# Kernel optimization log

Hardware: AMD Instinct MI355X
Metric: run time of the kernel (lower is better)

## Reference

```python
import jax, jax.numpy as jnp
import numpy as np

B, N, E, H, KVC = 2, 1024, 512, 8, 1536  # KVC = 3*E, head_dim = E//H = 64
EPS = 1e-5  # torch InstanceNorm2d default eps


def instance_norm(x):
    # normalize over the last two (spatial) dims per (batch, channel); biased var, no affine
    mu = jnp.mean(x, axis=(-2, -1), keepdims=True)
    var = jnp.var(x, axis=(-2, -1), keepdims=True)
    return (x - mu) * jax.lax.rsqrt(var + EPS)


def _heads(x):
    # [B, T, E] -> [B, H, T, E//H]
    b, t, e = x.shape
    return x.reshape(b, t, H, e // H).transpose(0, 2, 1, 3)


def setup_inputs() -> dict:
    key = jax.random.key(0)
    ks = jax.random.split(key, 16)
    s_e = 1.0 / np.sqrt(E)
    s_c = 1.0 / np.sqrt(KVC)
    inp = {
        'emb1': jax.random.normal(ks[0], (B, N, E), jnp.float32),
        'emb2': jax.random.normal(ks[1], (B, N, E), jnp.float32),
        'emb3': jax.random.normal(ks[2], (B, N, E), jnp.float32),
        'emb_C': jax.random.normal(ks[3], (B, N, KVC), jnp.float32),
        'Wq1': jax.random.normal(ks[4], (E, E), jnp.float32) * s_e,
        'Wq2': jax.random.normal(ks[5], (E, E), jnp.float32) * s_e,
        'Wq3': jax.random.normal(ks[6], (E, E), jnp.float32) * s_e,
        'Wk': jax.random.normal(ks[7], (E, E), jnp.float32) * s_e,
        'Wv': jax.random.normal(ks[8], (E, E), jnp.float32) * s_e,
        'WqC': jax.random.normal(ks[9], (KVC, KVC), jnp.float32) * s_c,
        'WkC': jax.random.normal(ks[10], (KVC, KVC), jnp.float32) * s_c,
        'WvC': jax.random.normal(ks[11], (KVC, KVC), jnp.float32) * s_c,
        'Wo1': jax.random.normal(ks[12], (E, E), jnp.float32) * s_e,
        'Wo2': jax.random.normal(ks[13], (E, E), jnp.float32) * s_e,
        'Wo3': jax.random.normal(ks[14], (E, E), jnp.float32) * s_e,
    }
    return inp


def reference(emb1, emb2, emb3, emb_C, Wq1, Wq2, Wq3, Wk, Wv, WqC, WkC, WvC, Wo1, Wo2, Wo3):
    # ---- channel attention over emb_C ----
    Q_C = emb_C @ WqC.T  # [B, N, KVC]
    K_C = emb_C @ WkC.T
    V_C = emb_C @ WvC.T
    attn_c = jnp.einsum('bnc,bnd->bcd', Q_C, K_C)          # [B, KVC, KVC]
    ch_sim = jax.nn.softmax(instance_norm(attn_c), axis=-1)  # psi1 (1 channel) + softmax(dim=3)
    ctx_c = jnp.einsum('bcd,bnd->bcn', ch_sim, V_C)        # [B, KVC, N]
    T_hat = ctx_c.transpose(0, 2, 1)                        # [B, N, KVC]
    # split last dim into 3 chunks of E, concat along token dim -> shared K/V source [B, 3N, E]
    KV_S = jnp.concatenate(jnp.split(T_hat, 3, axis=2), axis=1)

    # ---- spatial attention: 3 query streams share one K/V ----
    K = _heads(KV_S @ Wk.T)                # [B, H, 3N, d]
    V = _heads(KV_S @ Wv.T)                # [B, H, 3N, d]
    Kt = K.transpose(0, 1, 3, 2)           # [B, H, d, 3N]

    def stream(emb, Wq, Wo):
        Q = _heads(emb @ Wq.T)              # [B, H, N, d]
        attn = Q @ Kt                       # [B, H, N, 3N]
        sim = jax.nn.softmax(instance_norm(attn), axis=-1)  # psi2 per (b,h) + softmax
        ctx = sim @ V                       # [B, H, N, d]
        ctx = ctx.transpose(0, 2, 1, 3).reshape(emb.shape[0], emb.shape[1], E)
        return ctx @ Wo.T

    O1 = stream(emb1, Wq1, Wo1)
    O2 = stream(emb2, Wq2, Wo2)
    O3 = stream(emb3, Wq3, Wo3)
    return (O1, O2, O3)
```

## Files before the change

### kernel.cpp

```cpp
#include <hip/hip_runtime.h>
#include <math.h>

#define NTOK 1024
#define EDIM 512
#define KVCH 1536
#define TKV  3072
#define VSTRIDE 6144

typedef __bf16 bf16x8 __attribute__((ext_vector_type(8)));
typedef float f32x4 __attribute__((ext_vector_type(4)));
#define MFMA16(a,b,c) __builtin_amdgcn_mfma_f32_16x16x32_bf16(a,b,c,0,0,0)

__device__ __forceinline__ ushort f2bf(float f){
    uint u = __float_as_uint(f);
    u += 0x7FFFu + ((u>>16)&1u);
    return (ushort)(u>>16);
}
__device__ __forceinline__ float bf2f(ushort h){ return __uint_as_float(((uint)h)<<16); }
__device__ __forceinline__ bf16x8 ldsb8(const ushort* p){ return *(const bf16x8*)p; }

__device__ __forceinline__ void async16(const ushort* g, ushort* l){
    __builtin_amdgcn_global_load_lds((const __attribute__((address_space(1))) void*)g,
                                     (__attribute__((address_space(3))) void*)l, 16, 0, 0);
}

#define NCVT 15
struct CvtJobs { const float* src[NCVT]; ushort* hi[NCVT]; ushort* lo[NCVT]; int n[NCVT]; };

__global__ __launch_bounds__(256) void cvt_hilo(CvtJobs J)
{
    int a = blockIdx.y;
    int i = (blockIdx.x*256 + threadIdx.x)*4;
    if (i >= J.n[a]) return;
    float4 v = *(const float4*)(J.src[a] + i);
    ushort4 h, l;
    h.x=f2bf(v.x); l.x=f2bf(v.x-bf2f(h.x));
    h.y=f2bf(v.y); l.y=f2bf(v.y-bf2f(h.y));
    h.z=f2bf(v.z); l.z=f2bf(v.z-bf2f(h.z));
    h.w=f2bf(v.w); l.w=f2bf(v.w-bf2f(h.w));
    *(ushort4*)(J.hi[a]+i) = h;
    *(ushort4*)(J.lo[a]+i) = l;
}

struct GemmDesc {
    const ushort *Ahi, *Alo, *Bhi, *Blo;
    float* Cf; ushort *Chi, *Clo, *Cthi, *Ctlo;
    double* stats;
    int K, lda, ldb, ldc, ldct;
    int zmod;
    long sA0, sA1, sB0, sB1, sC0, sC1;
};

__device__ __forceinline__ void stage_ab(const ushort* hi, const ushort* lo, int ld, int k0,
                                         ushort* lds, int wave, int lane)
{
    #pragma unroll
    for (int i=0;i<4;++i){
        int r = (i<<5) + (wave<<3) + (lane>>3);
        int g = (lane&7) ^ (r&7);
        const ushort* s = ((g&4) ? lo : hi) + (size_t)r*ld + k0 + ((g&3)<<3);
        async16(s, lds + (((i<<5) + (wave<<3))<<6));
    }
}

__global__ __launch_bounds__(256) void mgemmF(GemmDesc D0, GemmDesc D1,
                                              int nblk0, int nx0, int ny0, int nx1, int ny1)
{
    __shared__ ushort A2[2][8192], B2[2][8192];
    __shared__ double sred[8];
    const int tid = threadIdx.x;
    int bid = blockIdx.x;
    GemmDesc d; int nx, ny, rel;
    if (bid < nblk0) { d = D0; rel = bid; nx = nx0; ny = ny0; }
    else             { d = D1; rel = bid - nblk0; nx = nx1; ny = ny1; }
    const int bx = rel % nx; int tt = rel / nx;
    const int by = tt % ny;  const int z = tt / ny;
    const int zb = z / d.zmod, zj = z - zb*d.zmod;
    const int mb = by<<7, nb = bx<<7;
    const ushort* Ah = d.Ahi + (size_t)zb*d.sA0 + (size_t)zj*d.sA1 + (size_t)mb*d.lda;
    const ushort* Al = d.Alo + (size_t)zb*d.sA0 + (size_t)zj*d.sA1 + (size_t)mb*d.lda;
    const ushort* Bh = d.Bhi + (size_t)zb*d.sB0 + (size_t)zj*d.sB1 + (size_t)nb*d.ldb;
    const ushort* Bl = d.Blo + (size_t)zb*d.sB0 + (size_t)zj*d.sB1 + (size_t)nb*d.ldb;
    const size_t coff = (size_t)zb*d.sC0 + (size_t)zj*d.sC1;
    const int wave = tid>>6, lane = tid&63;
    const int wr = wave>>1, wc = wave&1;
    const int fr = lane&15, fq = lane>>4;
    f32x4 acc[4][4];
    #pragma unroll
    for (int i=0;i<4;++i)
        #pragma unroll
        for (int j=0;j<4;++j) acc[i][j] = (f32x4){0.f,0.f,0.f,0.f};

    stage_ab(Ah, Al, d.lda, 0, A2[0], wave, lane);
    stage_ab(Bh, Bl, d.ldb, 0, B2[0], wave, lane);
    __syncthreads();
    int cur = 0;
    for (int k0=0; k0<d.K; k0+=32) {
        if (k0+32 < d.K) {
            stage_ab(Ah, Al, d.lda, k0+32, A2[cur^1], wave, lane);
            stage_ab(Bh, Bl, d.ldb, k0+32, B2[cur^1], wave, lane);
        }
        bf16x8 fah[4], fal[4];
        #pragma unroll
        for (int m=0;m<4;++m) {
            int r = wr*64 + m*16 + fr;
            const ushort* base = &A2[cur][r<<6];
            fah[m] = ldsb8(base + ((fq ^ (r&7))<<3));
            fal[m] = ldsb8(base + (((fq|4) ^ (r&7))<<3));
        }
        #pragma unroll
        for (int n=0;n<4;++n) {
            int r = wc*64 + n*16 + fr;
            const ushort* base = &B2[cur][r<<6];
            bf16x8 fbh = ldsb8(base + ((fq ^ (r&7))<<3));
            bf16x8 fbl = ldsb8(base + (((fq|4) ^ (r&7))<<3));
            #pragma unroll
            for (int m=0;m<4;++m) {
                acc[m][n] = MFMA16(fah[m], fbh, acc[m][n]);
                acc[m][n] = MFMA16(fah[m], fbl, acc[m][n]);
                acc[m][n] = MFMA16(fal[m], fbh, acc[m][n]);
            }
        }
        __syncthreads();
        cur ^= 1;
    }
    #pragma unroll
    for (int m=0;m<4;++m) {
        #pragma unroll
        for (int n=0;n<4;++n) {
            int row = mb + wr*64 + m*16 + fq*4;
            int col = nb + wc*64 + n*16 + fr;
            f32x4 v = acc[m][n];
            if (d.Cf) {
                #pragma unroll
                for (int r=0;r<4;++r) d.Cf[coff + (size_t)(row+r)*d.ldc + col] = v[r];
            }
            if (d.Chi) {
                #pragma unroll
                for (int r=0;r<4;++r) {
                    ushort hh = f2bf(v[r]);
                    size_t o = coff + (size_t)(row+r)*d.ldc + col;
                    d.Chi[o] = hh; d.Clo[o] = f2bf(v[r]-bf2f(hh));
                }
            }
            if (d.Cthi) {
                ushort4 h4, l4;
                #pragma unroll
                for (int r=0;r<4;++r) {
                    ushort hh = f2bf(v[r]);
                    ((ushort*)&h4)[r] = hh;
                    ((ushort*)&l4)[r] = f2bf(v[r]-bf2f(hh));
                }
                size_t o = coff + (size_t)col*d.ldct + row;
                *(ushort4*)(d.Cthi+o) = h4;
                *(ushort4*)(d.Ctlo+o) = l4;
            }
        }
    }
    if (d.stats) {
        double s=0.0, s2=0.0;
        #pragma unroll
        for (int m=0;m<4;++m)
            #pragma unroll
            for (int n=0;n<4;++n)
                #pragma unroll
                for (int r=0;r<4;++r) { double v = acc[m][n][r]; s += v; s2 += v*v; }
        #pragma unroll
        for (int off=32; off; off>>=1) { s += __shfl_xor(s, off); s2 += __shfl_xor(s2, off); }
        if (lane==0){ sred[wave]=s; sred[4+wave]=s2; }
        __syncthreads();
        if (tid==0) {
            atomicAdd(&d.stats[2*zb],   sred[0]+sred[1]+sred[2]+sred[3]);
            atomicAdd(&d.stats[2*zb+1], sred[4]+sred[5]+sred[6]+sred[7]);
        }
    }
}

__global__ __launch_bounds__(256) void chan_softmax(const float* __restrict__ ATT, const double* __restrict__ ST,
                                                    ushort* __restrict__ Shi, ushort* __restrict__ Slo)
{
    int b = blockIdx.y;
    size_t ro = (size_t)b * KVCH * KVCH + (size_t)blockIdx.x * KVCH;
    const float* p = ATT + ro;
    ushort* ph = Shi + ro;
    ushort* pl = Slo + ro;
    double cnt = (double)KVCH * (double)KVCH;
    double mean = ST[2*b] / cnt;
    double var  = ST[2*b+1] / cnt - mean * mean;
    float sc = (float)(1.0 / sqrt(var + 1e-5));
    int tid = threadIdx.x;
    float x[6];
    #pragma unroll
    for (int k = 0; k < 6; ++k) x[k] = p[tid + (k << 8)] * sc;
    float mx = fmaxf(fmaxf(fmaxf(x[0],x[1]),fmaxf(x[2],x[3])),fmaxf(x[4],x[5]));
    #pragma unroll
    for (int m = 32; m; m >>= 1) mx = fmaxf(mx, __shfl_xor(mx, m));
    __shared__ float red[4];
    int w = tid >> 6;
    if ((tid & 63) == 0) red[w] = mx;
    __syncthreads();
    mx = fmaxf(fmaxf(red[0],red[1]), fmaxf(red[2],red[3]));
    __syncthreads();
    float e[6]; float sum = 0.f;
    #pragma unroll
    for (int k = 0; k < 6; ++k) { e[k] = __expf(x[k] - mx); sum += e[k]; }
    #pragma unroll
    for (int m = 32; m; m >>= 1) sum += __shfl_xor(sum, m);
    if ((tid & 63) == 0) red[w] = sum;
    __syncthreads();
    sum = red[0]+red[1]+red[2]+red[3];
    float inv = 1.0f / sum;
    #pragma unroll
    for (int k = 0; k < 6; ++k) {
        float pv = e[k] * inv;
        ushort hh = f2bf(pv);
        ph[tid + (k << 8)] = hh;
        pl[tid + (k << 8)] = f2bf(pv - bf2f(hh));
    }
}

__global__ __launch_bounds__(256) void gram4(
    const ushort* __restrict__ Kbhi, const ushort* __restrict__ Kblo,
    const ushort* __restrict__ QBhi, const ushort* __restrict__ QBlo,
    float* __restrict__ GK, float* __restrict__ SK,
    float* __restrict__ GQ, float* __restrict__ SQm)
{
    int z = blockIdx.z;
    const ushort *Xh, *Xl; int T; float *G, *CS;
    if (z == 0) { Xh=Kbhi; Xl=Kblo; T=TKV; G=GK; CS=SK; }
    else { Xh=QBhi+(size_t)(z-1)*1048576; Xl=QBlo+(size_t)(z-1)*1048576;
           T=NTOK; G=GQ+(size_t)(z-1)*65536; CS=SQm+(size_t)(z-1)*1024; }
    int bh = blockIdx.x;
    int b = bh >> 3, h = bh & 7;
    const ushort* Xbh = Xh + (size_t)b * T * EDIM + h * 64;
    const ushort* Xbl = Xl + (size_t)b * T * EDIM + h * 64;
    int rows = T / gridDim.y;
    int t0 = blockIdx.y * rows;
    __shared__ float Xs[4][64];
    int tid = threadIdx.x;
    int i0 = (tid >> 4) << 2, j0 = (tid & 15) << 2;
    float acc[4][4] = {};
    float cs = 0.f;
    for (int t = t0; t < t0 + rows; t += 4) {
        __syncthreads();
        int r = tid >> 6, c = tid & 63;
        size_t gidx = (size_t)(t + r) * EDIM + c;
        Xs[r][c] = bf2f(Xbh[gidx]) + bf2f(Xbl[gidx]);
        __syncthreads();
        #pragma unroll
        for (int rr = 0; rr < 4; ++rr) {
            float xi0=Xs[rr][i0], xi1=Xs[rr][i0+1], xi2=Xs[rr][i0+2], xi3=Xs[rr][i0+3];
            float xj0=Xs[rr][j0], xj1=Xs[rr][j0+1], xj2=Xs[rr][j0+2], xj3=Xs[rr][j0+3];
            acc[0][0]=fmaf(xi0,xj0,acc[0][0]); acc[0][1]=fmaf(xi0,xj1,acc[0][1]); acc[0][2]=fmaf(xi0,xj2,acc[0][2]); acc[0][3]=fmaf(xi0,xj3,acc[0][3]);
            acc[1][0]=fmaf(xi1,xj0,acc[1][0]); acc[1][1]=fmaf(xi1,xj1,acc[1][1]); acc[1][2]=fmaf(xi1,xj2,acc[1][2]); acc[1][3]=fmaf(xi1,xj3,acc[1][3]);
            acc[2][0]=fmaf(xi2,xj0,acc[2][0]); acc[2][1]=fmaf(xi2,xj1,acc[2][1]); acc[2][2]=fmaf(xi2,xj2,acc[2][2]); acc[2][3]=fmaf(xi2,xj3,acc[2][3]);
            acc[3][0]=fmaf(xi3,xj0,acc[3][0]); acc[3][1]=fmaf(xi3,xj1,acc[3][1]); acc[3][2]=fmaf(xi3,xj2,acc[3][2]); acc[3][3]=fmaf(xi3,xj3,acc[3][3]);
        }
        if (tid < 64) cs += Xs[0][tid] + Xs[1][tid] + Xs[2][tid] + Xs[3][tid];
    }
    float* Gp = G + (size_t)bh * 4096;
    #pragma unroll
    for (int i = 0; i < 4; ++i)
        #pragma unroll
        for (int j = 0; j < 4; ++j)
            atomicAdd(&Gp[(i0 + i) * 64 + j0 + j], acc[i][j]);
    if (tid < 64) atomicAdd(&CS[bh * 64 + tid], cs);
}

__global__ __launch_bounds__(256) void spatial_scale(
    const float* __restrict__ GQ, const float* __restrict__ GK,
    const float* __restrict__ SQm, const float* __restrict__ SKm, float* __restrict__ SVo)
{
    int st = blockIdx.y, bh = blockIdx.x, tid = threadIdx.x;
    const float* gq = GQ + (size_t)st*65536 + bh*4096;
    const float* gk = GK + bh*4096;
    double e2 = 0.0;
    for (int i = tid; i < 4096; i += 256)
        e2 += (double)gq[i] * (double)gk[i];
    double mm = 0.0;
    if (tid < 64) mm = (double)SQm[(size_t)st*1024 + bh*64 + tid] * (double)SKm[bh*64 + tid];
    #pragma unroll
    for (int m = 32; m; m >>= 1) { e2 += __shfl_xor(e2, m); mm += __shfl_xor(mm, m); }
    __shared__ double se[4], sm[4];
    int w = tid >> 6;
    if ((tid & 63) == 0) { se[w] = e2; sm[w] = mm; }
    __syncthreads();
    if (tid == 0) {
        double cnt = (double)NTOK * (double)TKV;
        double E2 = (se[0]+se[1]+se[2]+se[3]) / cnt;
        double M  = (sm[0]+sm[1]+sm[2]+sm[3]) / cnt;
        double var = E2 - M * M;
        SVo[st*16+bh] = (float)(1.0 / sqrt(var + 1e-5));
    }
}

__global__ __launch_bounds__(256) void flash_mfma(
    const ushort* __restrict__ Qhi, const ushort* __restrict__ Qlo,
    const ushort* __restrict__ Khi, const ushort* __restrict__ Klo,
    const ushort* __restrict__ VThi, const ushort* __restrict__ VTlo,
    const float* __restrict__ SV,
    ushort* __restrict__ Ohi, ushort* __restrict__ Olo)
{
    __shared__ ushort Kh[2][4096], Kl[2][4096], Vh[2][4096], Vl[2][4096], Ph[4096];
    const int st = blockIdx.z, bh = blockIdx.y, b = bh>>3, h = bh&7;
    const int n0 = blockIdx.x<<6;
    const int tid = threadIdx.x, wave = tid>>6, lane = tid&63;
    const int fr = lane&15, fq = lane>>4;
    const float sc = SV[st*16 + bh];
    const size_t qb = (size_t)st*1048576 + (size_t)(b*1024 + n0)*512 + h*64;
    bf16x8 qfh[2], qfl[2];
    {
        const ushort* qph = Qhi + qb + (size_t)(wave*16 + fr)*512;
        const ushort* qpl = Qlo + qb + (size_t)(wave*16 + fr)*512;
        #pragma unroll
        for (int ks=0; ks<2; ++ks) {
            qfh[ks] = ldsb8(qph + ks*32 + fq*8);
            qfl[ks] = ldsb8(qpl + ks*32 + fq*8);
        }
    }
    f32x4 accO[4]; float lsum[4];
    #pragma unroll
    for (int i=0;i<4;++i){ accO[i]=(f32x4){0.f,0.f,0.f,0.f}; lsum[i]=0.f; }
    const size_t kb = (size_t)(b*TKV)*512 + h*64;
    const size_t vb = (size_t)(h*64)*VSTRIDE + b*TKV;

    auto stage_kv = [&](int tn, int buf){
        #pragma unroll
        for (int it=0; it<2; ++it) {
            int r  = (wave<<4) + (it<<3) + (lane>>3);
            int lb = ((wave<<4) + (it<<3)) << 6;
            int gck = ((lane&7) ^ (r&7)) << 3;
            size_t gk = kb + (size_t)(tn+r)*512 + gck;
            size_t gv = vb + (size_t)r*VSTRIDE + tn + gck;
            async16(Khi+gk, &Kh[buf][lb]);
            async16(Klo+gk, &Kl[buf][lb]);
            async16(VThi+gv, &Vh[buf][lb]);
            async16(VTlo+gv, &Vl[buf][lb]);
        }
    };

    stage_kv(0, 0);
    __syncthreads();
    int cur = 0;
    for (int t0=0; t0<TKV; t0+=64) {
        if (t0+64 < TKV) stage_kv(t0+64, cur^1);
        f32x4 s[4];
        #pragma unroll
        for (int i=0;i<4;++i) s[i]=(f32x4){0.f,0.f,0.f,0.f};
        #pragma unroll
        for (int ks=0; ks<2; ++ks) {
            #pragma unroll
            for (int nf=0; nf<4; ++nf) {
                int r = nf*16+fr;
                int ko = (r<<6) + ((ks*32 + fq*8) ^ ((r&7)<<3));
                bf16x8 kh = ldsb8(&Kh[cur][ko]), kl = ldsb8(&Kl[cur][ko]);
                s[nf] = MFMA16(qfh[ks], kh, s[nf]);
                s[nf] = MFMA16(qfh[ks], kl, s[nf]);
                s[nf] = MFMA16(qfl[ks], kh, s[nf]);
            }
        }
        #pragma unroll
        for (int reg=0; reg<4; ++reg) {
            int prow = fq*4+reg;
            float psum = 0.f;
            #pragma unroll
            for (int nf=0;nf<4;++nf){
                float p = __expf(sc * s[nf][reg]);
                psum += p;
                int pidx = (wave<<10) + (prow<<6) + ((nf*16+fr) ^ ((prow&7)<<3));
                Ph[pidx] = f2bf(p);
            }
            lsum[reg] += psum;
        }
        #pragma unroll
        for (int ks=0; ks<2; ++ks) {
            int po = (wave<<10) + (fr<<6) + ((ks*32 + fq*8) ^ ((fr&7)<<3));
            bf16x8 ph = ldsb8(&Ph[po]);
            #pragma unroll
            for (int df=0; df<4; ++df) {
                int dd = df*16+fr;
                int vo = (dd<<6) + ((ks*32 + fq*8) ^ ((dd&7)<<3));
                bf16x8 vh = ldsb8(&Vh[cur][vo]), vl = ldsb8(&Vl[cur][vo]);
                accO[df] = MFMA16(ph, vh, accO[df]);
                accO[df] = MFMA16(ph, vl, accO[df]);
            }
        }
        __syncthreads();
        cur ^= 1;
    }
    #pragma unroll
    for (int reg=0; reg<4; ++reg) {
        #pragma unroll
        for (int m=1; m<16; m<<=1) lsum[reg] += __shfl_xor(lsum[reg], m, 16);
        float inv = 1.f/lsum[reg];
        int row = n0 + wave*16 + fq*4 + reg;
        #pragma unroll
        for (int df=0; df<4; ++df) {
            float v = accO[df][reg]*inv;
            size_t o = (size_t)st*1048576 + (size_t)(b*1024+row)*512 + h*64 + df*16 + fr;
            ushort hh = f2bf(v);
            Ohi[o] = hh; Olo[o] = f2bf(v-bf2f(hh));
        }
    }
}

constexpr size_t OFF_CH  = 0;
constexpr size_t OFF_GK  = 64;
constexpr size_t OFF_SK  = 262208;
constexpr size_t OFF_GQ  = 266304;
constexpr size_t OFF_SQM = 1052736;
constexpr size_t OFF_SV  = 1065024;
constexpr size_t ZERO_BYTES = 1065024;
constexpr size_t S0 = 1065472;
constexpr size_t S1 = S0 + 8388608;
constexpr size_t S2 = S1 + 28311552;
constexpr size_t S3 = S2 + 12582912;
constexpr size_t S4 = S3 + 12582912;
constexpr size_t S5 = S4 + 12582912;
constexpr size_t S6 = S5 + 12582912;

extern "C" void kernel_launch(void* const* d_in, const int* in_sizes, int n_in,
                              void* d_out, int out_size, void* d_ws, size_t ws_size,
                              hipStream_t stream)
{
    const float* emb[3] = {(const float*)d_in[0], (const float*)d_in[1], (const float*)d_in[2]};
    const float* embC = (const float*)d_in[3];
    const float* WqF[3] = {(const float*)d_in[4], (const float*)d_in[5], (const float*)d_in[6]};
    const float* WkF  = (const float*)d_in[7];
    const float* WvF  = (const float*)d_in[8];
    const float* WCF[3] = {(const float*)d_in[9], (const float*)d_in[10], (const float*)d_in[11]};
    const float* WoF[3] = {(const float*)d_in[12], (const float*)d_in[13], (const float*)d_in[14]};
    float* out = (float*)d_out;
    char* ws = (char*)d_ws;

    auto U16 = [&](size_t off)->ushort* { return (ushort*)(ws + off); };
    auto F32 = [&](size_t off)->float*  { return (float*)(ws + off); };

    double* CH = (double*)(ws + OFF_CH);
    float *GK = F32(OFF_GK), *SK = F32(OFF_SK), *GQ = F32(OFF_GQ), *SQm = F32(OFF_SQM), *SV = F32(OFF_SV);

    auto W8hi = [&](int i){ return U16(S0 + (size_t)i*1048576); };
    auto W8lo = [&](int i){ return U16(S0 + (size_t)i*1048576 + 524288); };
    auto WChi = [&](int i){ return U16(S1 + (size_t)i*9437184); };
    auto WClo = [&](int i){ return U16(S1 + (size_t)i*9437184 + 4718592); };
    ushort *embChi=U16(S2), *embClo=U16(S2+6291456);
    ushort *embhi=U16(S3), *emblo=U16(S3+6291456);
    ushort *QCthi=U16(S4), *QCtlo=U16(S4+6291456);
    ushort *KCthi=U16(S5), *KCtlo=U16(S5+6291456);
    ushort *VChi=U16(S6), *VClo=U16(S6+6291456);
    float  *ATT = F32(S1);
    ushort *SIMhi=U16(S4), *SIMlo=U16(S4+9437184);
    ushort *KVShi=U16(S2), *KVSlo=U16(S2+6291456);
    ushort *QBhi=U16(S1), *QBlo=U16(S1+6291456);
    ushort *Kbhi=U16(S1+12582912), *Kblo=U16(S1+12582912+6291456);
    ushort *VThi=U16(S6), *VTlo=U16(S6+6291456);
    ushort *CTXhi=U16(S5), *CTXlo=U16(S5+6291456);

    dim3 blk(256);
    (void)hipMemsetAsync(d_ws, 0, ZERO_BYTES, stream);

    CvtJobs J;
    J.src[0]=embC;   J.hi[0]=embChi; J.lo[0]=embClo; J.n[0]=2048*KVCH;
    for (int s=0;s<3;++s){ J.src[1+s]=emb[s]; J.hi[1+s]=embhi+(size_t)s*1048576; J.lo[1+s]=emblo+(size_t)s*1048576; J.n[1+s]=2*NTOK*EDIM; }
    for (int s=0;s<3;++s){ J.src[4+s]=WqF[s]; J.hi[4+s]=W8hi(s); J.lo[4+s]=W8lo(s); J.n[4+s]=EDIM*EDIM; }
    J.src[7]=WkF; J.hi[7]=W8hi(3); J.lo[7]=W8lo(3); J.n[7]=EDIM*EDIM;
    J.src[8]=WvF; J.hi[8]=W8hi(4); J.lo[8]=W8lo(4); J.n[8]=EDIM*EDIM;
    for (int s=0;s<3;++s){ J.src[9+s]=WCF[s]; J.hi[9+s]=WChi(s); J.lo[9+s]=WClo(s); J.n[9+s]=KVCH*KVCH; }
    for (int s=0;s<3;++s){ J.src[12+s]=WoF[s]; J.hi[12+s]=W8hi(5+s); J.lo[12+s]=W8lo(5+s); J.n[12+s]=EDIM*EDIM; }
    cvt_hilo<<<dim3(3072, NCVT), blk, 0, stream>>>(J);

    GemmDesc Z{}; Z.zmod = 1;

    {
        GemmDesc dq = Z;
        dq.Ahi=embChi; dq.Alo=embClo; dq.Bhi=WChi(0); dq.Blo=WClo(0);
        dq.Cthi=QCthi; dq.Ctlo=QCtlo;
        dq.K=KVCH; dq.lda=KVCH; dq.ldb=KVCH; dq.ldct=NTOK;
        dq.zmod=2; dq.sA0=0; dq.sA1=(long)NTOK*KVCH; dq.sB0=4718592; dq.sB1=0;
        dq.sC0=6291456; dq.sC1=(long)KVCH*NTOK;
        GemmDesc dv = Z;
        dv.Ahi=embChi; dv.Alo=embClo; dv.Bhi=WChi(2); dv.Blo=WClo(2);
        dv.Chi=VChi; dv.Clo=VClo;
        dv.K=KVCH; dv.lda=KVCH; dv.ldb=KVCH; dv.ldc=KVCH;
        dv.sA0=(long)NTOK*KVCH; dv.sC0=(long)NTOK*KVCH;
        mgemmF<<<dim3(576), blk, 0, stream>>>(dq, dv, 384, 12, 8, 12, 8);
    }
    {
        GemmDesc da = Z;
        da.Ahi=QCthi; da.Alo=QCtlo; da.Bhi=KCthi; da.Blo=KCtlo;
        da.Cf=ATT; da.stats=CH;
        da.K=NTOK; da.lda=NTOK; da.ldb=NTOK; da.ldc=KVCH;
        da.sA0=(long)KVCH*NTOK; da.sB0=(long)KVCH*NTOK; da.sC0=(long)KVCH*KVCH;
        mgemmF<<<dim3(288), blk, 0, stream>>>(da, da, 288, 12, 12, 1, 1);
    }
    chan_softmax<<<dim3(1536,2), blk, 0, stream>>>(ATT, CH, SIMhi, SIMlo);
    {
        GemmDesc dk = Z;
        dk.Ahi=VChi; dk.Alo=VClo; dk.Bhi=SIMhi; dk.Blo=SIMlo;
        dk.Chi=KVShi; dk.Clo=KVSlo;
        dk.K=KVCH; dk.lda=KVCH; dk.ldb=KVCH; dk.ldc=EDIM;
        dk.zmod=3; dk.sA0=(long)NTOK*KVCH; dk.sA1=0;
        dk.sB0=(long)KVCH*KVCH; dk.sB1=(long)EDIM*KVCH;
        dk.sC0=(long)TKV*EDIM; dk.sC1=(long)NTOK*EDIM;
        GemmDesc dqp = Z;
        dqp.Ahi=embhi; dqp.Alo=emblo; dqp.Bhi=W8hi(0); dqp.Blo=W8lo(0);
        dqp.Chi=QBhi; dqp.Clo=QBlo;
        dqp.K=EDIM; dqp.lda=EDIM; dqp.ldb=EDIM; dqp.ldc=EDIM;
        dqp.sA0=1048576; dqp.sB0=524288; dqp.sC0=1048576;
        mgemmF<<<dim3(384), blk, 0, stream>>>(dk, dqp, 192, 4, 8, 4, 16);
    }
    {
        GemmDesc dkp = Z;
        dkp.Ahi=KVShi; dkp.Alo=KVSlo; dkp.Bhi=W8hi(3); dkp.Blo=W8lo(3);
        dkp.Chi=Kbhi; dkp.Clo=Kblo;
        dkp.K=EDIM; dkp.lda=EDIM; dkp.ldb=EDIM; dkp.ldc=EDIM;
        GemmDesc dvp = Z;
        dvp.Ahi=KVShi; dvp.Alo=KVSlo; dvp.Bhi=W8hi(4); dvp.Blo=W8lo(4);
        dvp.Cthi=VThi; dvp.Ctlo=VTlo;
        dvp.K=EDIM; dvp.lda=EDIM; dvp.ldb=EDIM; dvp.ldct=VSTRIDE;
        mgemmF<<<dim3(384), blk, 0, stream>>>(dkp, dvp, 192, 4, 48, 4, 48);
    }
    gram4<<<dim3(16,8,4), blk, 0, stream>>>(Kbhi, Kblo, QBhi, QBlo, GK, SK, GQ, SQm);
    spatial_scale<<<dim3(16,3), blk, 0, stream>>>(GQ, GK, SQm, SK, SV);
    flash_mfma<<<dim3(16,16,3), blk, 0, stream>>>(QBhi, QBlo, Kbhi, Kblo, VThi, VTlo, SV, CTXhi, CTXlo);
    {
        GemmDesc dop = Z;
        dop.Ahi=CTXhi; dop.Alo=CTXlo; dop.Bhi=W8hi(5); dop.Blo=W8lo(5);
        dop.Cf=out;
        dop.K=EDIM; dop.lda=EDIM; dop.ldb=EDIM; dop.ldc=EDIM;
        dop.sA0=1048576; dop.sB0=524288; dop.sC0=1048576;
        mgemmF<<<dim3(192), blk, 0, stream>>>(dop, dop, 192, 4, 16, 1, 1);
    }
}
```

Baseline: 684.0 us.

## Single-buffer flash KV tiles, remap blocks per XCD, raise MFMA wave priority

The flash attention kernel drops its double-buffered K/V LDS staging for a single buffer with a barrier after each load. This halves LDS use so more blocks can be resident per CU, and relies on occupancy rather than software prefetch to hide load latency. The grid becomes 1-D and is remapped so that blocks landing on the same XCD share the same (stream, batch, head) K/V data, which is meant to improve L2 reuse. s_setprio is raised around the MFMA sections in both the flash and GEMM kernels. In exchange, loads inside each block are no longer overlapped with compute.

```diff
diff --git a/kernel.cpp b/kernel.cpp
--- a/kernel.cpp
+++ b/kernel.cpp
@@ -108,6 +108,7 @@
             fah[m] = ldsb8(base + ((fq ^ (r&7))<<3));
             fal[m] = ldsb8(base + (((fq|4) ^ (r&7))<<3));
         }
+        __builtin_amdgcn_s_setprio(1);
         #pragma unroll
         for (int n=0;n<4;++n) {
             int r = wc*64 + n*16 + fr;
@@ -121,6 +122,7 @@
                 acc[m][n] = MFMA16(fal[m], fbh, acc[m][n]);
             }
         }
+        __builtin_amdgcn_s_setprio(0);
         __syncthreads();
         cur ^= 1;
     }
@@ -301,9 +303,13 @@
     const float* __restrict__ SV,
     ushort* __restrict__ Ohi, ushort* __restrict__ Olo)
 {
-    __shared__ ushort Kh[2][4096], Kl[2][4096], Vh[2][4096], Vl[2][4096], Ph[4096];
-    const int st = blockIdx.z, bh = blockIdx.y, b = bh>>3, h = bh&7;
-    const int n0 = blockIdx.x<<6;
+    __shared__ ushort Kh[4096], Kl[4096], Vh[4096], Vl[4096], Ph[4096];
+    const int g = blockIdx.x;
+    const int xcd = g & 7, loc = g >> 3;
+    const int sbh = xcd*6 + (loc >> 4);
+    const int st = sbh >> 4, bh = sbh & 15;
+    const int b = bh>>3, h = bh&7;
+    const int n0 = (loc & 15) << 6;
     const int tid = threadIdx.x, wave = tid>>6, lane = tid&63;
     const int fr = lane&15, fq = lane>>4;
     const float sc = SV[st*16 + bh];
@@ -323,42 +329,37 @@
     for (int i=0;i<4;++i){ accO[i]=(f32x4){0.f,0.f,0.f,0.f}; lsum[i]=0.f; }
     const size_t kb = (size_t)(b*TKV)*512 + h*64;
     const size_t vb = (size_t)(h*64)*VSTRIDE + b*TKV;
-
-    auto stage_kv = [&](int tn, int buf){
+    for (int t0=0; t0<TKV; t0+=64) {
         #pragma unroll
         for (int it=0; it<2; ++it) {
             int r  = (wave<<4) + (it<<3) + (lane>>3);
             int lb = ((wave<<4) + (it<<3)) << 6;
             int gck = ((lane&7) ^ (r&7)) << 3;
-            size_t gk = kb + (size_t)(tn+r)*512 + gck;
-            size_t gv = vb + (size_t)r*VSTRIDE + tn + gck;
-            async16(Khi+gk, &Kh[buf][lb]);
-            async16(Klo+gk, &Kl[buf][lb]);
-            async16(VThi+gv, &Vh[buf][lb]);
-            async16(VTlo+gv, &Vl[buf][lb]);
-        }
-    };
-
-    stage_kv(0, 0);
-    __syncthreads();
-    int cur = 0;
-    for (int t0=0; t0<TKV; t0+=64) {
-        if (t0+64 < TKV) stage_kv(t0+64, cur^1);
+            size_t gk = kb + (size_t)(t0+r)*512 + gck;
+            size_t gv = vb + (size_t)r*VSTRIDE + t0 + gck;
+            async16(Khi+gk, &Kh[lb]);
+            async16(Klo+gk, &Kl[lb]);
+            async16(VThi+gv, &Vh[lb]);
+            async16(VTlo+gv, &Vl[lb]);
+        }
+        __syncthreads();
         f32x4 s[4];
         #pragma unroll
         for (int i=0;i<4;++i) s[i]=(f32x4){0.f,0.f,0.f,0.f};
+        __builtin_amdgcn_s_setprio(1);
         #pragma unroll
         for (int ks=0; ks<2; ++ks) {
             #pragma unroll
             for (int nf=0; nf<4; ++nf) {
                 int r = nf*16+fr;
                 int ko = (r<<6) + ((ks*32 + fq*8) ^ ((r&7)<<3));
-                bf16x8 kh = ldsb8(&Kh[cur][ko]), kl = ldsb8(&Kl[cur][ko]);
+                bf16x8 kh = ldsb8(&Kh[ko]), kl = ldsb8(&Kl[ko]);
                 s[nf] = MFMA16(qfh[ks], kh, s[nf]);
                 s[nf] = MFMA16(qfh[ks], kl, s[nf]);
                 s[nf] = MFMA16(qfl[ks], kh, s[nf]);
             }
         }
+        __builtin_amdgcn_s_setprio(0);
         #pragma unroll
         for (int reg=0; reg<4; ++reg) {
             int prow = fq*4+reg;
@@ -372,6 +373,7 @@
             }
             lsum[reg] += psum;
         }
+        __builtin_amdgcn_s_setprio(1);
         #pragma unroll
         for (int ks=0; ks<2; ++ks) {
             int po = (wave<<10) + (fr<<6) + ((ks*32 + fq*8) ^ ((fr&7)<<3));
@@ -380,13 +382,13 @@
             for (int df=0; df<4; ++df) {
                 int dd = df*16+fr;
                 int vo = (dd<<6) + ((ks*32 + fq*8) ^ ((dd&7)<<3));
-                bf16x8 vh = ldsb8(&Vh[cur][vo]), vl = ldsb8(&Vl[cur][vo]);
+                bf16x8 vh = ldsb8(&Vh[vo]), vl = ldsb8(&Vl[vo]);
                 accO[df] = MFMA16(ph, vh, accO[df]);
                 accO[df] = MFMA16(ph, vl, accO[df]);
             }
         }
+        __builtin_amdgcn_s_setprio(0);
         __syncthreads();
-        cur ^= 1;
     }
     #pragma unroll
     for (int reg=0; reg<4; ++reg) {
@@ -522,7 +524,7 @@
     }
     gram4<<<dim3(16,8,4), blk, 0, stream>>>(Kbhi, Kblo, QBhi, QBlo, GK, SK, GQ, SQm);
     spatial_scale<<<dim3(16,3), blk, 0, stream>>>(GQ, GK, SQm, SK, SV);
-    flash_mfma<<<dim3(16,16,3), blk, 0, stream>>>(QBhi, QBlo, Kbhi, Kblo, VThi, VTlo, SV, CTXhi, CTXlo);
+    flash_mfma<<<dim3(768), blk, 0, stream>>>(QBhi, QBlo, Kbhi, Kblo, VThi, VTlo, SV, CTXhi, CTXlo);
     {
         GemmDesc dop = Z;
         dop.Ahi=CTXhi; dop.Alo=CTXlo; dop.Bhi=W8hi(5); dop.Blo=W8lo(5);
```

Result: faster. 639.4 us (-6.5%).
